# Kernel tuning notes

Hardware: AMD Instinct MI355X
Metric: run time of the kernel (lower is better)

## Reference

```python
import jax, jax.numpy as jnp
import numpy as np

B, S, DIM = 4, 2048, 1024
H, HD = 16, 64
MB = 16
NMB = S // MB
DEG, CP = 3, 8
NB = CP + DEG  # 11 basis functions
NKNOTS = CP + 1 + 2 * DEG  # 15
EPS = 1e-6
BASE_LR = 1.0


def bspline(x, knots, degree=DEG):
    # Cox-de Boor recursion; x: (...,), knots: (G,) uniform -> (..., G-1-degree)
    xk = x[..., None]
    G = knots.shape[0]
    b = ((xk >= knots[:-1]) & (xk < knots[1:])).astype(x.dtype)
    for k in range(1, degree + 1):
        left = (xk - knots[: G - 1 - k]) / (knots[k: G - 1] - knots[: G - 1 - k])
        right = (knots[k + 1: G] - xk) / (knots[k + 1: G] - knots[1: G - k])
        b = left * b[..., :-1] + right * b[..., 1:]
    return b


def ln_fwd(x, gamma, beta, eps=EPS):
    mu = x.mean(-1, keepdims=True)
    var = ((x - mu) ** 2).mean(-1, keepdims=True)
    x_hat = (x - mu) / jnp.sqrt(var + eps)
    return gamma * x_hat + beta


def ln_fused_l2_bwd(x, l2_target, gamma, beta, eps=EPS):
    mu = x.mean(-1, keepdims=True)
    var = ((x - mu) ** 2).mean(-1, keepdims=True)
    std = jnp.sqrt(var + eps)
    x_hat = (x - mu) / std
    grad_x_hat = (gamma * x_hat + beta - l2_target) * gamma
    z = (grad_x_hat - grad_x_hat.mean(-1, keepdims=True)
         - x_hat * (grad_x_hat * x_hat).mean(-1, keepdims=True)) / std
    return z


def apply_rope(t, ang):
    # t: (B,H,S,hd), ang: (S, hd//2) rotation angles
    cos, sin = jnp.cos(ang), jnp.sin(ang)
    t1, t2 = t[..., 0::2], t[..., 1::2]
    r1 = t1 * cos - t2 * sin
    r2 = t1 * sin + t2 * cos
    return jnp.stack([r1, r2], axis=-1).reshape(t.shape)


def setup_inputs() -> dict:
    key = jax.random.key(0)
    ks = jax.random.split(key, 8)
    s = 0.02
    x = jax.random.normal(ks[0], (B, S, DIM), dtype=jnp.float32)
    inv_freq = 1.0 / (10000.0 ** (jnp.arange(0, HD, 2, dtype=jnp.float32) / HD))
    pos_frequencies = jnp.arange(S, dtype=jnp.float32)[:, None] * inv_freq[None, :]
    Wq = jax.random.normal(ks[1], (DIM, DIM), dtype=jnp.float32) * s
    Wk = jax.random.normal(ks[2], (DIM, DIM), dtype=jnp.float32) * s
    Wv = jax.random.normal(ks[3], (DIM, DIM), dtype=jnp.float32) * s
    Wo = jax.random.normal(ks[4], (DIM, DIM), dtype=jnp.float32) * s
    lr_W = jax.random.normal(ks[5], (H, 1, DIM), dtype=jnp.float32) * s
    lr_b = jnp.zeros((H, 1), dtype=jnp.float32)
    g_scale = jnp.zeros((MB,), dtype=jnp.float32)
    ttt_gamma = jnp.ones((H, HD), dtype=jnp.float32)
    ttt_beta = jnp.zeros((H, HD), dtype=jnp.float32)
    post_w = jnp.ones((DIM,), dtype=jnp.float32)
    post_b = jnp.zeros((DIM,), dtype=jnp.float32)
    knots = jnp.linspace(-1.0, 1.0, NKNOTS, dtype=jnp.float32)
    coefficients = jax.random.normal(ks[6], (H, NB, HD), dtype=jnp.float32) * s
    return dict(x=x, pos_frequencies=pos_frequencies, Wq=Wq, Wk=Wk, Wv=Wv, Wo=Wo,
                lr_W=lr_W, lr_b=lr_b, g_scale=g_scale, ttt_gamma=ttt_gamma,
                ttt_beta=ttt_beta, post_w=post_w, post_b=post_b,
                coefficients=coefficients, knots=knots)


def reference(x, pos_frequencies, Wq, Wk, Wv, Wo, lr_W, lr_b, g_scale,
              ttt_gamma, ttt_beta, post_w, post_b, coefficients, knots):
    Bx, Sx = x.shape[:2]
    proj = lambda W: (x @ W.T).reshape(Bx, Sx, H, HD).transpose(0, 2, 1, 3)
    Q = apply_rope(proj(Wq), pos_frequencies)
    K = apply_rope(proj(Wk), pos_frequencies)
    V = apply_rope(proj(Wv), pos_frequencies)

    to_mb = lambda t: t.reshape(Bx, H, NMB, MB, HD).transpose(2, 0, 1, 3, 4)
    Qm, Km, Vm = to_mb(Q), to_mb(K), to_mb(V)  # (n,B,H,m,hd)

    # inner-loop learning rates (get_learning_rate)
    x4 = x.reshape(Bx, NMB, MB, DIM)
    lr = BASE_LR * jax.nn.sigmoid(
        jnp.einsum('bnkd,hd->bhnk', x4, lr_W[:, 0, :]) + lr_b.reshape(1, H, 1, 1)) / HD
    gs = jnp.clip(1.0 / jnp.arange(1, MB + 1, dtype=x.dtype) + g_scale, 0.0, None)
    eta = (lr * gs).transpose(2, 0, 1, 3)  # (n,B,H,m)

    gamma = ttt_gamma[None, :, None, :]
    beta = ttt_beta[None, :, None, :]
    W0 = jnp.broadcast_to(coefficients, (Bx, H, NB, HD))

    def step(W, inp):
        Qi, Ki, Vi, ei = inp  # (B,H,m,hd), eta (B,H,m)
        basK = bspline(Ki, knots)                      # (B,H,m,hd,nb)
        Zk = jax.nn.silu(Ki) + jnp.einsum('bhmdn,bhnd->bhmd', basK, W)
        gz = ln_fused_l2_bwd(Zk, Vi - Ki, gamma, beta)  # (B,H,m,hd)
        tok = jnp.einsum('bhm,bhmd,bhmdn->bhmnd', ei, gz, basK)
        cum = jnp.cumsum(tok, axis=2)                  # causal coeff-grad (B,H,m,nb,hd)
        basQ = bspline(Qi, knots)
        Zq = (jax.nn.silu(Qi)
              + jnp.einsum('bhmdn,bhnd->bhmd', basQ, W)
              - jnp.einsum('bhmdn,bhmnd->bhmd', basQ, cum))
        y = Qi + ln_fwd(Zq, gamma, beta)
        return W - cum[:, :, -1], y

    _, ys = jax.lax.scan(step, W0, (Qm, Km, Vm, eta))  # ys: (n,B,H,m,hd)
    out = ys.transpose(1, 0, 3, 2, 4).reshape(Bx, Sx, DIM)

    mu = out.mean(-1, keepdims=True)
    var = ((out - mu) ** 2).mean(-1, keepdims=True)
    out = (out - mu) / jnp.sqrt(var + EPS) * post_w + post_b
    return out @ Wo.T
```

## Files before the change

kernel.cpp:

```cpp
#include <hip/hip_runtime.h>
#include <stdint.h>


typedef unsigned short ushort_t;
typedef _Float16 f16x8 __attribute__((ext_vector_type(8)));
typedef float f32x4 __attribute__((ext_vector_type(4)));

__device__ __forceinline__ float fast_silu(float x) {
    const float e = __builtin_amdgcn_exp2f(-1.4426950408889634f * x);
    return x * __builtin_amdgcn_rcpf(1.0f + e);
}
__device__ __forceinline__ float fast_rsq(float x) {
    return __builtin_amdgcn_rsqf(x);
}

__device__ __forceinline__ void gl16(const ushort_t* g, ushort_t* l) {
    __builtin_amdgcn_global_load_lds(
        (const __attribute__((address_space(1))) void*)g,
        (__attribute__((address_space(3))) void*)l, 16, 0, 0);
}

template <int CTRL>
__device__ __forceinline__ float dpp_add(float v) {
    int p = __builtin_amdgcn_update_dpp(0, __float_as_int(v), CTRL, 0xF, 0xF, false);
    return v + __int_as_float(p);
}
__device__ __forceinline__ float wave_sum(float v) {
    v = dpp_add<0xB1>(v);
    v = dpp_add<0x4E>(v);
    v = dpp_add<0x141>(v);
    v = dpp_add<0x140>(v);
    v = dpp_add<0x142>(v);
    v = dpp_add<0x143>(v);
    return __int_as_float(__builtin_amdgcn_readlane(__float_as_int(v), 63));
}

__device__ __forceinline__ float rdl63(float v) {
    return __int_as_float(__builtin_amdgcn_readlane(__float_as_int(v), 63));
}

__device__ __forceinline__ void wave_sum6(float& s0, float& s1, float& s2,
                                          float& s3, float& s4, float& s5) {
    asm volatile(
        "s_nop 1\n\t"
        "v_add_f32_dpp %0, %0, %0 quad_perm:[1,0,3,2] row_mask:0xf bank_mask:0xf\n\t"
        "v_add_f32_dpp %1, %1, %1 quad_perm:[1,0,3,2] row_mask:0xf bank_mask:0xf\n\t"
        "v_add_f32_dpp %2, %2, %2 quad_perm:[1,0,3,2] row_mask:0xf bank_mask:0xf\n\t"
        "v_add_f32_dpp %3, %3, %3 quad_perm:[1,0,3,2] row_mask:0xf bank_mask:0xf\n\t"
        "v_add_f32_dpp %4, %4, %4 quad_perm:[1,0,3,2] row_mask:0xf bank_mask:0xf\n\t"
        "v_add_f32_dpp %5, %5, %5 quad_perm:[1,0,3,2] row_mask:0xf bank_mask:0xf\n\t"
        "v_add_f32_dpp %0, %0, %0 quad_perm:[2,3,0,1] row_mask:0xf bank_mask:0xf\n\t"
        "v_add_f32_dpp %1, %1, %1 quad_perm:[2,3,0,1] row_mask:0xf bank_mask:0xf\n\t"
        "v_add_f32_dpp %2, %2, %2 quad_perm:[2,3,0,1] row_mask:0xf bank_mask:0xf\n\t"
        "v_add_f32_dpp %3, %3, %3 quad_perm:[2,3,0,1] row_mask:0xf bank_mask:0xf\n\t"
        "v_add_f32_dpp %4, %4, %4 quad_perm:[2,3,0,1] row_mask:0xf bank_mask:0xf\n\t"
        "v_add_f32_dpp %5, %5, %5 quad_perm:[2,3,0,1] row_mask:0xf bank_mask:0xf\n\t"
        "v_add_f32_dpp %0, %0, %0 row_half_mirror row_mask:0xf bank_mask:0xf\n\t"
        "v_add_f32_dpp %1, %1, %1 row_half_mirror row_mask:0xf bank_mask:0xf\n\t"
        "v_add_f32_dpp %2, %2, %2 row_half_mirror row_mask:0xf bank_mask:0xf\n\t"
        "v_add_f32_dpp %3, %3, %3 row_half_mirror row_mask:0xf bank_mask:0xf\n\t"
        "v_add_f32_dpp %4, %4, %4 row_half_mirror row_mask:0xf bank_mask:0xf\n\t"
        "v_add_f32_dpp %5, %5, %5 row_half_mirror row_mask:0xf bank_mask:0xf\n\t"
        "v_add_f32_dpp %0, %0, %0 row_mirror row_mask:0xf bank_mask:0xf\n\t"
        "v_add_f32_dpp %1, %1, %1 row_mirror row_mask:0xf bank_mask:0xf\n\t"
        "v_add_f32_dpp %2, %2, %2 row_mirror row_mask:0xf bank_mask:0xf\n\t"
        "v_add_f32_dpp %3, %3, %3 row_mirror row_mask:0xf bank_mask:0xf\n\t"
        "v_add_f32_dpp %4, %4, %4 row_mirror row_mask:0xf bank_mask:0xf\n\t"
        "v_add_f32_dpp %5, %5, %5 row_mirror row_mask:0xf bank_mask:0xf\n\t"
        "v_add_f32_dpp %0, %0, %0 row_bcast:15 row_mask:0xf bank_mask:0xf bound_ctrl:0\n\t"
        "v_add_f32_dpp %1, %1, %1 row_bcast:15 row_mask:0xf bank_mask:0xf bound_ctrl:0\n\t"
        "v_add_f32_dpp %2, %2, %2 row_bcast:15 row_mask:0xf bank_mask:0xf bound_ctrl:0\n\t"
        "v_add_f32_dpp %3, %3, %3 row_bcast:15 row_mask:0xf bank_mask:0xf bound_ctrl:0\n\t"
        "v_add_f32_dpp %4, %4, %4 row_bcast:15 row_mask:0xf bank_mask:0xf bound_ctrl:0\n\t"
        "v_add_f32_dpp %5, %5, %5 row_bcast:15 row_mask:0xf bank_mask:0xf bound_ctrl:0\n\t"
        "v_add_f32_dpp %0, %0, %0 row_bcast:31 row_mask:0xf bank_mask:0xf bound_ctrl:0\n\t"
        "v_add_f32_dpp %1, %1, %1 row_bcast:31 row_mask:0xf bank_mask:0xf bound_ctrl:0\n\t"
        "v_add_f32_dpp %2, %2, %2 row_bcast:31 row_mask:0xf bank_mask:0xf bound_ctrl:0\n\t"
        "v_add_f32_dpp %3, %3, %3 row_bcast:31 row_mask:0xf bank_mask:0xf bound_ctrl:0\n\t"
        "v_add_f32_dpp %4, %4, %4 row_bcast:31 row_mask:0xf bank_mask:0xf bound_ctrl:0\n\t"
        "v_add_f32_dpp %5, %5, %5 row_bcast:31 row_mask:0xf bank_mask:0xf bound_ctrl:0"
        : "+v"(s0), "+v"(s1), "+v"(s2), "+v"(s3), "+v"(s4), "+v"(s5));
}

__device__ __forceinline__ void wave_sum2(float& s0, float& s1) {
    asm volatile(
        "s_nop 1\n\t"
        "v_add_f32_dpp %0, %0, %0 quad_perm:[1,0,3,2] row_mask:0xf bank_mask:0xf\n\t"
        "v_add_f32_dpp %1, %1, %1 quad_perm:[1,0,3,2] row_mask:0xf bank_mask:0xf\n\t"
        "s_nop 0\n\t"
        "v_add_f32_dpp %0, %0, %0 quad_perm:[2,3,0,1] row_mask:0xf bank_mask:0xf\n\t"
        "v_add_f32_dpp %1, %1, %1 quad_perm:[2,3,0,1] row_mask:0xf bank_mask:0xf\n\t"
        "s_nop 0\n\t"
        "v_add_f32_dpp %0, %0, %0 row_half_mirror row_mask:0xf bank_mask:0xf\n\t"
        "v_add_f32_dpp %1, %1, %1 row_half_mirror row_mask:0xf bank_mask:0xf\n\t"
        "s_nop 0\n\t"
        "v_add_f32_dpp %0, %0, %0 row_mirror row_mask:0xf bank_mask:0xf\n\t"
        "v_add_f32_dpp %1, %1, %1 row_mirror row_mask:0xf bank_mask:0xf\n\t"
        "s_nop 0\n\t"
        "v_add_f32_dpp %0, %0, %0 row_bcast:15 row_mask:0xf bank_mask:0xf bound_ctrl:0\n\t"
        "v_add_f32_dpp %1, %1, %1 row_bcast:15 row_mask:0xf bank_mask:0xf bound_ctrl:0\n\t"
        "s_nop 0\n\t"
        "v_add_f32_dpp %0, %0, %0 row_bcast:31 row_mask:0xf bank_mask:0xf bound_ctrl:0\n\t"
        "v_add_f32_dpp %1, %1, %1 row_bcast:31 row_mask:0xf bank_mask:0xf bound_ctrl:0"
        : "+v"(s0), "+v"(s1));
}

struct Bas4 { float n[4]; int row; };
__device__ __forceinline__ Bas4 bspline4(float x) {
    const float xp1 = x + 1.0f;
    const float s7 = xp1 * 7.0f;
    const float fi = floorf(s7);
    const bool valid = (fi >= 0.0f) && (fi <= 13.0f);
    const float fic = valid ? fi : 0.0f;
    const float t = s7 - fic;
    const float u = 1.0f - t;
    const float t2 = t * t;
    const float t3 = t2 * t;
    const float u3 = u * u * u;
    const float N0 = u3 * 0.16666666666666666f;
    const float N3 = t3 * 0.16666666666666666f;
    const float N1 = fmaf(0.5f, t3, 0.66666666666666666f - t2);
    const float N2 = 1.0f - N0 - N1 - N3;

    Bas4 r;
    const int i = (int)fic;
    const float nv[4] = {N0, N1, N2, N3};
#pragma unroll
    for (int tt = 0; tt < 4; ++tt) {
        const int j = i + tt - 3;
        const bool ok = valid && ((unsigned)j <= 10u);
        r.n[tt] = ok ? nv[tt] : 0.0f;
    }
    r.row = i;
    return r;
}

__device__ __forceinline__ void split16_body(
    const float* __restrict__ in, ushort_t* __restrict__ hi,
    ushort_t* __restrict__ lo, int i)
{
    const float4 f = reinterpret_cast<const float4*>(in)[i];
    union { _Float16 h[4]; ushort4 u; } hv, lv;
    hv.h[0] = (_Float16)f.x; hv.h[1] = (_Float16)f.y;
    hv.h[2] = (_Float16)f.z; hv.h[3] = (_Float16)f.w;
    lv.h[0] = (_Float16)(f.x - (float)hv.h[0]);
    lv.h[1] = (_Float16)(f.y - (float)hv.h[1]);
    lv.h[2] = (_Float16)(f.z - (float)hv.h[2]);
    lv.h[3] = (_Float16)(f.w - (float)hv.h[3]);
    reinterpret_cast<ushort4*>(hi)[i] = hv.u;
    reinterpret_cast<ushort4*>(lo)[i] = lv.u;
}

__device__ __forceinline__ void cast16_body(
    const float* __restrict__ in, ushort_t* __restrict__ out, int i)
{
    const float4 f = reinterpret_cast<const float4*>(in)[i];
    union { _Float16 h[4]; ushort4 u; } cv;
    cv.h[0] = (_Float16)f.x; cv.h[1] = (_Float16)f.y;
    cv.h[2] = (_Float16)f.z; cv.h[3] = (_Float16)f.w;
    reinterpret_cast<ushort4*>(out)[i] = cv.u;
}

__global__ __launch_bounds__(256) void prep_kernel(
    const float* __restrict__ x,
    const float* __restrict__ Wq, const float* __restrict__ Wk,
    const float* __restrict__ Wv,
    const float* __restrict__ lrW, const float* __restrict__ lrb,
    const float* __restrict__ gsc, const float* __restrict__ posf,
    ushort_t* __restrict__ xh, ushort_t* __restrict__ xl,
    ushort_t* __restrict__ Wq16, ushort_t* __restrict__ Wk16,
    ushort_t* __restrict__ Wv16,
    float* __restrict__ eta, float2* __restrict__ rtab)
{
    const int bid = blockIdx.x;
    const int tid = threadIdx.x;
    if (bid < 8192) {
        split16_body(x, xh, xl, bid * 256 + tid);
    } else if (bid < 9216) {
        cast16_body(Wq, Wq16, (bid - 8192) * 256 + tid);
    } else if (bid < 10240) {
        cast16_body(Wk, Wk16, (bid - 9216) * 256 + tid);
    } else if (bid < 11264) {
        cast16_body(Wv, Wv16, (bid - 10240) * 256 + tid);
    } else if (bid < 13312) {
        const int row = (bid - 11264) * 4 + (tid >> 6);
        const int lane = tid & 63;
        float xv[16];
#pragma unroll
        for (int i = 0; i < 16; ++i) xv[i] = x[(size_t)row * 1024 + lane + i * 64];
        const int b = row >> 11, s = row & 2047, n = s >> 4, m = s & 15;
        const float gs = fmaxf(1.0f / (float)(m + 1) + gsc[m], 0.0f);
        for (int h = 0; h < 16; ++h) {
            float acc = 0.0f;
#pragma unroll
            for (int i = 0; i < 16; ++i) acc += xv[i] * lrW[h * 1024 + lane + i * 64];
            acc = wave_sum(acc);
            if (lane == 0) {
                float sig = 1.0f / (1.0f + expf(-(acc + lrb[h])));
                eta[(((size_t)(b * 16 + h)) * 128 + n) * 16 + m] = (sig / 64.0f) * gs;
            }
        }
    } else {
        const int i = (bid - 13312) * 256 + tid;
        const float ang = posf[i];
        rtab[i] = make_float2(cosf(ang), sinf(ang));
    }
}

__global__ __launch_bounds__(256) void cast16_kernel(
    const float* __restrict__ in, ushort_t* __restrict__ out, int n4)
{
    const int i = blockIdx.x * 256 + threadIdx.x;
    if (i >= n4) return;
    cast16_body(in, out, i);
}

#define RAW_BAR()                                                              \
    __builtin_amdgcn_s_barrier();                                              \
    asm volatile("" ::: "memory");

__global__ __launch_bounds__(512) void qkv_rope_kernel(
    const ushort_t* __restrict__ xh, const ushort_t* __restrict__ xl,
    const ushort_t* __restrict__ Wq16, const ushort_t* __restrict__ Wk16,
    const ushort_t* __restrict__ Wv16,
    const float2* __restrict__ tab,
    float* __restrict__ Qb, float* __restrict__ Kb, float* __restrict__ Vb)
{
    const int cid = blockIdx.y * 64 + blockIdx.x;
    const int swz = (cid & 7) * 192 + (cid >> 3);
    const int rowbase = (swz & 63) * 128;
    const int colbase = (swz >> 6) * 128;
    const int sel = colbase >> 10;
    const ushort_t* WB = (sel == 0) ? Wq16 : (sel == 1) ? Wk16 : Wv16;
    float* dst = (sel == 0) ? Qb : (sel == 1) ? Kb : Vb;
    const int colm = colbase & 1023;

    __shared__ __align__(16) ushort_t Ash[3][4096];
    __shared__ __align__(16) ushort_t Asl[3][4096];
    __shared__ __align__(16) ushort_t Bsh[3][4096];
    const int tid = threadIdx.x;
    const int wv = tid >> 6, ln = tid & 63;
    const int l15 = ln & 15, lq = ln >> 4;
    const int lsw = lq ^ ((l15 >> 1) & 3);
    const int wm = wv >> 2, wn = wv & 3;
    const int srow = tid >> 2;
    const int skseg = (((tid & 3) ^ ((srow >> 1) & 3)) * 8);
    const ushort_t* gA_h = xh + (size_t)(rowbase + srow) * 1024 + skseg;
    const ushort_t* gA_l = xl + (size_t)(rowbase + srow) * 1024 + skseg;
    const ushort_t* gB   = WB + (size_t)(colm + srow) * 1024 + skseg;
    const int wlds = wv * 512;
    f32x4 acc[4][2] = {};

    ushort_t *cAh = &Ash[0][0], *cAl = &Asl[0][0], *cB = &Bsh[0][0];
    ushort_t *nAh = &Ash[1][0], *nAl = &Asl[1][0], *nB = &Bsh[1][0];
    ushort_t *pAh = &Ash[2][0], *pAl = &Asl[2][0], *pB = &Bsh[2][0];

    gl16(gA_h + 0,  cAh + wlds); gl16(gA_l + 0,  cAl + wlds); gl16(gB + 0,  cB + wlds);
    gl16(gA_h + 32, nAh + wlds); gl16(gA_l + 32, nAl + wlds); gl16(gB + 32, nB + wlds);

    for (int p = 0; p < 32; ++p) {
        const int kn = (p + 2) * 32;
        if (kn < 1024) {
            gl16(gA_h + kn, pAh + wlds);
            gl16(gA_l + kn, pAl + wlds);
            gl16(gB + kn,   pB + wlds);
            asm volatile("s_waitcnt vmcnt(6)" ::: "memory");
        } else if (p == 30) {
            asm volatile("s_waitcnt vmcnt(3)" ::: "memory");
        } else {
            asm volatile("s_waitcnt vmcnt(0)" ::: "memory");
        }
        RAW_BAR()
        {
            f16x8 bh[2];
#pragma unroll
            for (int u = 0; u < 2; ++u) {
                const int br = (wn * 32 + u * 16 + l15) * 32 + lsw * 8;
                bh[u] = *reinterpret_cast<const f16x8*>(&cB[br]);
            }
#pragma unroll
            for (int t = 0; t < 4; ++t) {
                const int ar = (wm * 64 + t * 16 + l15) * 32 + lsw * 8;
                const f16x8 ah = *reinterpret_cast<const f16x8*>(&cAh[ar]);
                const f16x8 al = *reinterpret_cast<const f16x8*>(&cAl[ar]);
#pragma unroll
                for (int u = 0; u < 2; ++u) {
                    acc[t][u] = __builtin_amdgcn_mfma_f32_16x16x32_f16(ah, bh[u], acc[t][u], 0, 0, 0);
                    acc[t][u] = __builtin_amdgcn_mfma_f32_16x16x32_f16(al, bh[u], acc[t][u], 0, 0, 0);
                }
            }
        }
        RAW_BAR()
        ushort_t* t0;
        t0 = cAh; cAh = nAh; nAh = pAh; pAh = t0;
        t0 = cAl; cAl = nAl; nAl = pAl; pAl = t0;
        t0 = cB;  cB  = nB;  nB  = pB;  pB  = t0;
    }

#pragma unroll
    for (int t = 0; t < 4; ++t)
#pragma unroll
        for (int u = 0; u < 2; ++u) {
            const int col = colm + wn * 32 + u * 16 + l15;
            const int d = col & 63, h = col >> 6;
            const int angidx = d >> 1;
            const int odd = d & 1;
#pragma unroll
            for (int r = 0; r < 4; ++r) {
                const int row = rowbase + wm * 64 + t * 16 + lq * 4 + r;
                const int b = row >> 11, s = row & 2047;
                const float2 cs = tab[s * 32 + angidx];
                const float own = acc[t][u][r];
                const float partner = __shfl_xor(own, 1, 64);
                const float res = odd ? (partner * cs.y + own * cs.x)
                                      : (own * cs.x - partner * cs.y);
                const int n = s >> 4, m = s & 15;
                dst[(((size_t)(b * 16 + h)) * 128 + n) * 1024 + m * 64 + d] = res;
            }
        }
}

__global__ __launch_bounds__(1024) void scan_kernel(
    const float* __restrict__ Qb, const float* __restrict__ Kb,
    const float* __restrict__ Vb, const float* __restrict__ eta,
    const float* __restrict__ tg, const float* __restrict__ tb,
    const float* __restrict__ coeff, float* __restrict__ out_pre)
{
    __shared__ __align__(16) float Wl[17 * 64];
    __shared__ __align__(16) float cum[16 * 17 * 64];
    __shared__ __align__(16) float Ucum[16 * 17 * 64];

    const int tid = threadIdx.x;
    const int m = tid >> 6, d = tid & 63;
    const int b = blockIdx.x >> 4, h = blockIdx.x & 15;

    const float gam = tg[h * 64 + d];
    const float bet = tb[h * 64 + d];
    const float gam2 = gam * gam;
    const float G = wave_sum(gam2);

    for (int i = tid; i < 1088; i += 1024)
        Wl[i] = (i >= 192 && i < 896) ? coeff[h * 704 + (i - 192)] : 0.0f;
    {
        const float4 z = {0.0f, 0.0f, 0.0f, 0.0f};
        float4* c4 = (float4*)cum;
        float4* u4 = (float4*)Ucum;
        for (int i = tid; i < 4352; i += 1024) { c4[i] = z; u4[i] = z; }
    }
    __syncthreads();

    const size_t base = ((size_t)(b * 16 + h)) * 131072;
    const float* Qp = Qb + base;
    const float* Kp = Kb + base;
    const float* Vp = Vb + base;
    const float* ep = eta + ((size_t)(b * 16 + h)) * 2048;

    float kf = Kp[tid], vf = Vp[tid], qf = Qp[tid], ei = ep[m];
    int rprev = 0;
    const int cb = m * 1088 + d;

    Bas4 bk = bspline4(kf);
    float szk = fast_silu(kf);
    float E = gam * (bet - (vf - kf));

    for (int n = 0; n < 128; ++n) {
        const int n1 = (n < 127) ? n + 1 : n;
        const float kfN = Kp[n1 * 1024 + tid];
        const float vfN = Vp[n1 * 1024 + tid];
        const float qfN = Qp[n1 * 1024 + tid];
        const float eiN = ep[n1 * 16 + m];

        float zk = szk;
        {
            const float* w = &Wl[bk.row * 64 + d];
            zk = fmaf(bk.n[0], w[0],   zk);
            zk = fmaf(bk.n[1], w[64],  zk);
            zk = fmaf(bk.n[2], w[128], zk);
            zk = fmaf(bk.n[3], w[192], zk);
        }

        float s0 = zk, s1 = zk * zk, s2 = gam2 * zk,
              s3 = gam2 * (zk * zk), s4 = E, s5 = E * zk;
        wave_sum6(s0, s1, s2, s3, s4, s5);
        const float r0 = rdl63(s0);
        const float r1 = rdl63(s1);
        const float r2 = rdl63(s2);
        const float r3 = rdl63(s3);
        const float r4 = rdl63(s4);
        const float r5 = rdl63(s5);

        const float mu = r0 * (1.0f / 64.0f);
        const float var = r1 * (1.0f / 64.0f) - mu * mu;
        const float rstd = fast_rsq(var + 1e-6f);
        const float xhat = (zk - mu) * rstd;
        const float gxh = gam2 * xhat + E;
        const float t1 = rstd * (r2 - mu * G) + r4;
        const float t2 = rstd * rstd * (r3 - 2.0f * mu * r2 + mu * mu * G)
                       + rstd * (r5 - mu * r4);
        const float gz = (gxh - t1 * (1.0f / 64.0f) - xhat * (t2 * (1.0f / 64.0f))) * rstd;

        const float tokf = ei * gz;
        {
            float* cz = &cum[cb + rprev * 64];
            cz[0] = 0.0f; cz[64] = 0.0f; cz[128] = 0.0f; cz[192] = 0.0f;
            float* cw = &cum[cb + bk.row * 64];
            cw[0]   = tokf * bk.n[0];
            cw[64]  = tokf * bk.n[1];
            cw[128] = tokf * bk.n[2];
            cw[192] = tokf * bk.n[3];
            rprev = bk.row;
        }
        __syncthreads();

        if (tid < 176) {
            float4* c4 = (float4*)cum;
            float4* u4 = (float4*)Ucum;
            float4* w4 = (float4*)Wl;
            float4 v[16];
#pragma unroll
            for (int mm = 0; mm < 16; ++mm) v[mm] = c4[mm * 272 + 48 + tid];
            float4 a = w4[48 + tid];
#pragma unroll
            for (int mm = 0; mm < 16; ++mm) {
                a.x -= v[mm].x; a.y -= v[mm].y; a.z -= v[mm].z; a.w -= v[mm].w;
                u4[mm * 272 + 48 + tid] = a;
            }
            w4[48 + tid] = a;
        }
        const Bas4 bq = bspline4(qf);
        float zq = fast_silu(qf);
        const Bas4 bkN = bspline4(kfN);
        const float szkN = fast_silu(kfN);
        const float EN = gam * (bet - (vfN - kfN));
        __syncthreads();

        {
            const float* u = &Ucum[cb + bq.row * 64];
            zq = fmaf(bq.n[0], u[0],   zq);
            zq = fmaf(bq.n[1], u[64],  zq);
            zq = fmaf(bq.n[2], u[128], zq);
            zq = fmaf(bq.n[3], u[192], zq);
        }

        float q0 = zq, q1 = zq * zq;
        wave_sum2(q0, q1);
        const float u1 = rdl63(q0);
        const float u2 = rdl63(q1);
        const float mu2 = u1 * (1.0f / 64.0f);
        const float var2 = u2 * (1.0f / 64.0f) - mu2 * mu2;
        const float rstd2 = fast_rsq(var2 + 1e-6f);
        const float y = qf + gam * (zq - mu2) * rstd2 + bet;
        out_pre[((size_t)b * 2048 + n * 16 + m) * 1024 + h * 64 + d] = y;

        kf = kfN; vf = vfN; qf = qfN; ei = eiN;
        bk = bkN; szk = szkN; E = EN;
    }
}

__global__ __launch_bounds__(256) void ln_kernel(
    const float* __restrict__ in, const float* __restrict__ pw,
    const float* __restrict__ pb, ushort_t* __restrict__ o16)
{
    const int row = blockIdx.x * 4 + (threadIdx.x >> 6);
    const int lane = threadIdx.x & 63;
    const float* r = in + (size_t)row * 1024;
    float v[16];
    float s1 = 0.0f, s2 = 0.0f;
#pragma unroll
    for (int i = 0; i < 16; ++i) {
        v[i] = r[lane + i * 64];
        s1 += v[i];
        s2 += v[i] * v[i];
    }
    s1 = wave_sum(s1);
    s2 = wave_sum(s2);
    const float mu = s1 * (1.0f / 1024.0f);
    const float var = s2 * (1.0f / 1024.0f) - mu * mu;
    const float rstd = rsqrtf(var + 1e-6f);
#pragma unroll
    for (int i = 0; i < 16; ++i) {
        const int c = lane + i * 64;
        const float o = (v[i] - mu) * rstd * pw[c] + pb[c];
        union { _Float16 h; ushort_t u; } cv;
        cv.h = (_Float16)o;
        o16[(size_t)row * 1024 + c] = cv.u;
    }
}

__global__ __launch_bounds__(512) void out_gemm_kernel(
    const ushort_t* __restrict__ Ag, const ushort_t* __restrict__ Bg,
    float* __restrict__ out)
{
    const int cid = blockIdx.y * 64 + blockIdx.x;
    const int swz = (cid & 7) * 64 + (cid >> 3);
    const int rowbase = (swz & 63) * 128;
    const int colbase = (swz >> 6) * 128;

    __shared__ __align__(16) ushort_t Ash[2][4096];
    __shared__ __align__(16) ushort_t Bsh[2][4096];
    const int tid = threadIdx.x;
    const int wv = tid >> 6, ln = tid & 63;
    const int l15 = ln & 15, lq = ln >> 4;
    const int lsw = lq ^ ((l15 >> 1) & 3);
    const int wm = wv >> 2, wn = wv & 3;
    const int srow = tid >> 2;
    const int skseg = (((tid & 3) ^ ((srow >> 1) & 3)) * 8);
    const ushort_t* gA = Ag + (size_t)(rowbase + srow) * 1024 + skseg;
    const ushort_t* gB = Bg + (size_t)(colbase + srow) * 1024 + skseg;
    const int wlds = wv * 512;
    f32x4 acc[4][2] = {};

#define OG_STAGE(B, KO)                                                        \
    gl16(gA + (KO), &Ash[B][wlds]);                                            \
    gl16(gB + (KO), &Bsh[B][wlds]);

#define OG_COMPUTE(B)                                                          \
    {                                                                          \
        f16x8 bh[2];                                                           \
        _Pragma("unroll")                                                      \
        for (int u = 0; u < 2; ++u) {                                          \
            const int br = (wn * 32 + u * 16 + l15) * 32 + lsw * 8;            \
            bh[u] = *reinterpret_cast<const f16x8*>(&Bsh[B][br]);              \
        }                                                                      \
        _Pragma("unroll")                                                      \
        for (int t = 0; t < 4; ++t) {                                          \
            const int ar = (wm * 64 + t * 16 + l15) * 32 + lsw * 8;            \
            const f16x8 ah = *reinterpret_cast<const f16x8*>(&Ash[B][ar]);     \
            _Pragma("unroll")                                                  \
            for (int u = 0; u < 2; ++u)                                        \
                acc[t][u] = __builtin_amdgcn_mfma_f32_16x16x32_f16(ah, bh[u], acc[t][u], 0, 0, 0); \
        }                                                                      \
    }

    OG_STAGE(0, 0)
    for (int k0 = 0; k0 < 1024; k0 += 64) {
        OG_STAGE(1, k0 + 32)
        asm volatile("s_waitcnt vmcnt(2)" ::: "memory");
        RAW_BAR()
        OG_COMPUTE(0)
        RAW_BAR()
        if (k0 + 64 < 1024) {
            OG_STAGE(0, k0 + 64)
            asm volatile("s_waitcnt vmcnt(2)" ::: "memory");
        } else {
            asm volatile("s_waitcnt vmcnt(0)" ::: "memory");
        }
        RAW_BAR()
        OG_COMPUTE(1)
        RAW_BAR()
    }
#undef OG_STAGE
#undef OG_COMPUTE

#pragma unroll
    for (int t = 0; t < 4; ++t)
#pragma unroll
        for (int u = 0; u < 2; ++u) {
            const int col = colbase + wn * 32 + u * 16 + l15;
#pragma unroll
            for (int r = 0; r < 4; ++r) {
                const int row = rowbase + wm * 64 + t * 16 + lq * 4 + r;
                out[(size_t)row * 1024 + col] = acc[t][u][r];
            }
        }
}

extern "C" void kernel_launch(void* const* d_in, const int* in_sizes, int n_in,
                              void* d_out, int out_size, void* d_ws, size_t ws_size,
                              hipStream_t stream) {
    const float* x    = (const float*)d_in[0];
    const float* posf = (const float*)d_in[1];
    const float* Wq   = (const float*)d_in[2];
    const float* Wk   = (const float*)d_in[3];
    const float* Wv   = (const float*)d_in[4];
    const float* Wo   = (const float*)d_in[5];
    const float* lrW  = (const float*)d_in[6];
    const float* lrb  = (const float*)d_in[7];
    const float* gsc  = (const float*)d_in[8];
    const float* tg   = (const float*)d_in[9];
    const float* tb   = (const float*)d_in[10];
    const float* pw   = (const float*)d_in[11];
    const float* pb   = (const float*)d_in[12];
    const float* coeff= (const float*)d_in[13];

    char* ws = (char*)d_ws;
    float*    Qb   = (float*)(ws);
    float*    Kb   = (float*)(ws + 33554432);
    float*    Vb   = (float*)(ws + 67108864);
    ushort_t* xh   = (ushort_t*)(ws + 100663296);
    ushort_t* xl   = (ushort_t*)(ws + 117440512);
    float*    outp = (float*)(ws + 100663296);
    float*    eta  = (float*)(ws + 134217728);
    ushort_t* Wq16 = (ushort_t*)(ws + 134742016);
    ushort_t* Wk16 = (ushort_t*)(ws + 136839168);
    ushort_t* Wv16 = (ushort_t*)(ws + 138936320);
    ushort_t* Wo16 = (ushort_t*)(ws + 147324928);
    ushort_t* ln16 = (ushort_t*)(ws);
    float2*   rtab = (float2*)(ws + 147324928);

    prep_kernel<<<13568, 256, 0, stream>>>(x, Wq, Wk, Wv, lrW, lrb, gsc, posf,
                                           xh, xl, Wq16, Wk16, Wv16, eta, rtab);
    qkv_rope_kernel<<<dim3(64, 24), 512, 0, stream>>>(xh, xl, Wq16, Wk16, Wv16,
                                                      rtab, Qb, Kb, Vb);
    cast16_kernel<<<1024, 256, 0, stream>>>(Wo, Wo16, 262144);
    scan_kernel<<<64, 1024, 0, stream>>>(Qb, Kb, Vb, eta, tg, tb, coeff, outp);
    ln_kernel<<<2048, 256, 0, stream>>>(outp, pw, pb, ln16);
    out_gemm_kernel<<<dim3(64, 8), 512, 0, stream>>>(ln16, Wo16, (float*)d_out);
}
```

Before: 537.0 us.

## Drop hi/lo split of x in QKV GEMM and use BK=64 double-buffered tiles

The QKV projection used to split x into fp16 hi and lo parts and issue two MFMAs per tile to keep near-fp32 accuracy. It now casts x to a single fp16 array, which halves the A-operand traffic and the MFMA count. Both the QKV and output GEMMs now share a double-buffered pipeline with a 64-wide K step and a new XOR swizzle, giving fewer barriers per K. The cost is lower precision in Q/K/V, which feed a recurrent scan where errors can compound, plus a change in LDS footprint.

```diff
diff --git a/kernel.cpp b/kernel.cpp
--- a/kernel.cpp
+++ b/kernel.cpp
@@ -135,22 +135,6 @@
     return r;
 }
 
-__device__ __forceinline__ void split16_body(
-    const float* __restrict__ in, ushort_t* __restrict__ hi,
-    ushort_t* __restrict__ lo, int i)
-{
-    const float4 f = reinterpret_cast<const float4*>(in)[i];
-    union { _Float16 h[4]; ushort4 u; } hv, lv;
-    hv.h[0] = (_Float16)f.x; hv.h[1] = (_Float16)f.y;
-    hv.h[2] = (_Float16)f.z; hv.h[3] = (_Float16)f.w;
-    lv.h[0] = (_Float16)(f.x - (float)hv.h[0]);
-    lv.h[1] = (_Float16)(f.y - (float)hv.h[1]);
-    lv.h[2] = (_Float16)(f.z - (float)hv.h[2]);
-    lv.h[3] = (_Float16)(f.w - (float)hv.h[3]);
-    reinterpret_cast<ushort4*>(hi)[i] = hv.u;
-    reinterpret_cast<ushort4*>(lo)[i] = lv.u;
-}
-
 __device__ __forceinline__ void cast16_body(
     const float* __restrict__ in, ushort_t* __restrict__ out, int i)
 {
@@ -167,7 +151,7 @@
     const float* __restrict__ Wv,
     const float* __restrict__ lrW, const float* __restrict__ lrb,
     const float* __restrict__ gsc, const float* __restrict__ posf,
-    ushort_t* __restrict__ xh, ushort_t* __restrict__ xl,
+    ushort_t* __restrict__ x16,
     ushort_t* __restrict__ Wq16, ushort_t* __restrict__ Wk16,
     ushort_t* __restrict__ Wv16,
     float* __restrict__ eta, float2* __restrict__ rtab)
@@ -175,7 +159,7 @@
     const int bid = blockIdx.x;
     const int tid = threadIdx.x;
     if (bid < 8192) {
-        split16_body(x, xh, xl, bid * 256 + tid);
+        cast16_body(x, x16, bid * 256 + tid);
     } else if (bid < 9216) {
         cast16_body(Wq, Wq16, (bid - 8192) * 256 + tid);
     } else if (bid < 10240) {
@@ -219,8 +203,61 @@
     __builtin_amdgcn_s_barrier();                                              \
     asm volatile("" ::: "memory");
 
+#define G2_DECLS()                                                             \
+    const int tid = threadIdx.x;                                               \
+    const int wv = tid >> 6, ln = tid & 63;                                    \
+    const int l15 = ln & 15, lq = ln >> 4, l7 = ln & 7;                        \
+    const int wm = wv >> 2, wn = wv & 3;                                       \
+    const int r8 = ln >> 3;                          \
+    const int gsw = (l7 ^ r8) * 8;                   \
+    const int a0d = (wv * 8) * 64;                 \
+    const int a1d = (64 + wv * 8) * 64;                                        \
+    f32x4 acc[4][2] = {};
+
+#define G2_STAGE(buf, KO)                                                      \
+    gl16(gA0 + (KO), &As[buf][a0d]);                                           \
+    gl16(gA1 + (KO), &As[buf][a1d]);                                           \
+    gl16(gB0 + (KO), &Bs[buf][a0d]);                                           \
+    gl16(gB1 + (KO), &Bs[buf][a1d]);
+
+#define G2_COMPUTE(buf)                                                        \
+    _Pragma("unroll")                                                          \
+    for (int ks = 0; ks < 2; ++ks) {                                           \
+        f16x8 bh[2];                                                           \
+        _Pragma("unroll")                                                      \
+        for (int u = 0; u < 2; ++u) {                                          \
+            const int br = (wn * 32 + u * 16 + l15) * 64                       \
+                         + ((((ks << 2) + lq) ^ l7) << 3);                     \
+            bh[u] = *reinterpret_cast<const f16x8*>(&Bs[buf][br]);             \
+        }                                                                      \
+        _Pragma("unroll")                                                      \
+        for (int t = 0; t < 4; ++t) {                                          \
+            const int ar = (wm * 64 + t * 16 + l15) * 64                       \
+                         + ((((ks << 2) + lq) ^ l7) << 3);                     \
+            const f16x8 ah = *reinterpret_cast<const f16x8*>(&As[buf][ar]);    \
+            _Pragma("unroll")                                                  \
+            for (int u = 0; u < 2; ++u)                                        \
+                acc[t][u] = __builtin_amdgcn_mfma_f32_16x16x32_f16(ah, bh[u], acc[t][u], 0, 0, 0); \
+        }                                                                      \
+    }
+
+#define G2_LOOP()                                                              \
+    G2_STAGE(0, 0)                                                             \
+    for (int p = 0; p < 16; ++p) {                                             \
+        const int buf = p & 1;                                                 \
+        if (p < 15) {                                                          \
+            G2_STAGE(buf ^ 1, (p + 1) * 64)                                    \
+            asm volatile("s_waitcnt vmcnt(4)" ::: "memory");                   \
+        } else {                                                               \
+            asm volatile("s_waitcnt vmcnt(0)" ::: "memory");                   \
+        }                                                                      \
+        RAW_BAR()                                                              \
+        G2_COMPUTE(buf)                                                        \
+        RAW_BAR()                                                              \
+    }
+
 __global__ __launch_bounds__(512) void qkv_rope_kernel(
-    const ushort_t* __restrict__ xh, const ushort_t* __restrict__ xl,
+    const ushort_t* __restrict__ x16,
     const ushort_t* __restrict__ Wq16, const ushort_t* __restrict__ Wk16,
     const ushort_t* __restrict__ Wv16,
     const float2* __restrict__ tab,
@@ -235,67 +272,15 @@
     float* dst = (sel == 0) ? Qb : (sel == 1) ? Kb : Vb;
     const int colm = colbase & 1023;
 
-    __shared__ __align__(16) ushort_t Ash[3][4096];
-    __shared__ __align__(16) ushort_t Asl[3][4096];
-    __shared__ __align__(16) ushort_t Bsh[3][4096];
-    const int tid = threadIdx.x;
-    const int wv = tid >> 6, ln = tid & 63;
-    const int l15 = ln & 15, lq = ln >> 4;
-    const int lsw = lq ^ ((l15 >> 1) & 3);
-    const int wm = wv >> 2, wn = wv & 3;
-    const int srow = tid >> 2;
-    const int skseg = (((tid & 3) ^ ((srow >> 1) & 3)) * 8);
-    const ushort_t* gA_h = xh + (size_t)(rowbase + srow) * 1024 + skseg;
-    const ushort_t* gA_l = xl + (size_t)(rowbase + srow) * 1024 + skseg;
-    const ushort_t* gB   = WB + (size_t)(colm + srow) * 1024 + skseg;
-    const int wlds = wv * 512;
-    f32x4 acc[4][2] = {};
-
-    ushort_t *cAh = &Ash[0][0], *cAl = &Asl[0][0], *cB = &Bsh[0][0];
-    ushort_t *nAh = &Ash[1][0], *nAl = &Asl[1][0], *nB = &Bsh[1][0];
-    ushort_t *pAh = &Ash[2][0], *pAl = &Asl[2][0], *pB = &Bsh[2][0];
-
-    gl16(gA_h + 0,  cAh + wlds); gl16(gA_l + 0,  cAl + wlds); gl16(gB + 0,  cB + wlds);
-    gl16(gA_h + 32, nAh + wlds); gl16(gA_l + 32, nAl + wlds); gl16(gB + 32, nB + wlds);
-
-    for (int p = 0; p < 32; ++p) {
-        const int kn = (p + 2) * 32;
-        if (kn < 1024) {
-            gl16(gA_h + kn, pAh + wlds);
-            gl16(gA_l + kn, pAl + wlds);
-            gl16(gB + kn,   pB + wlds);
-            asm volatile("s_waitcnt vmcnt(6)" ::: "memory");
-        } else if (p == 30) {
-            asm volatile("s_waitcnt vmcnt(3)" ::: "memory");
-        } else {
-            asm volatile("s_waitcnt vmcnt(0)" ::: "memory");
-        }
-        RAW_BAR()
-        {
-            f16x8 bh[2];
-#pragma unroll
-            for (int u = 0; u < 2; ++u) {
-                const int br = (wn * 32 + u * 16 + l15) * 32 + lsw * 8;
-                bh[u] = *reinterpret_cast<const f16x8*>(&cB[br]);
-            }
-#pragma unroll
-            for (int t = 0; t < 4; ++t) {
-                const int ar = (wm * 64 + t * 16 + l15) * 32 + lsw * 8;
-                const f16x8 ah = *reinterpret_cast<const f16x8*>(&cAh[ar]);
-                const f16x8 al = *reinterpret_cast<const f16x8*>(&cAl[ar]);
-#pragma unroll
-                for (int u = 0; u < 2; ++u) {
-                    acc[t][u] = __builtin_amdgcn_mfma_f32_16x16x32_f16(ah, bh[u], acc[t][u], 0, 0, 0);
-                    acc[t][u] = __builtin_amdgcn_mfma_f32_16x16x32_f16(al, bh[u], acc[t][u], 0, 0, 0);
-                }
-            }
-        }
-        RAW_BAR()
-        ushort_t* t0;
-        t0 = cAh; cAh = nAh; nAh = pAh; pAh = t0;
-        t0 = cAl; cAl = nAl; nAl = pAl; pAl = t0;
-        t0 = cB;  cB  = nB;  nB  = pB;  pB  = t0;
-    }
+    __shared__ __align__(16) ushort_t As[2][8192];
+    __shared__ __align__(16) ushort_t Bs[2][8192];
+    G2_DECLS()
+    const ushort_t* gA0 = x16 + (size_t)(rowbase + wv * 8 + r8) * 1024 + gsw;
+    const ushort_t* gA1 = gA0 + (size_t)64 * 1024;
+    const ushort_t* gB0 = WB + (size_t)(colm + wv * 8 + r8) * 1024 + gsw;
+    const ushort_t* gB1 = gB0 + (size_t)64 * 1024;
+
+    G2_LOOP()
 
 #pragma unroll
     for (int t = 0; t < 4; ++t)
@@ -496,61 +481,15 @@
     const int rowbase = (swz & 63) * 128;
     const int colbase = (swz >> 6) * 128;
 
-    __shared__ __align__(16) ushort_t Ash[2][4096];
-    __shared__ __align__(16) ushort_t Bsh[2][4096];
-    const int tid = threadIdx.x;
-    const int wv = tid >> 6, ln = tid & 63;
-    const int l15 = ln & 15, lq = ln >> 4;
-    const int lsw = lq ^ ((l15 >> 1) & 3);
-    const int wm = wv >> 2, wn = wv & 3;
-    const int srow = tid >> 2;
-    const int skseg = (((tid & 3) ^ ((srow >> 1) & 3)) * 8);
-    const ushort_t* gA = Ag + (size_t)(rowbase + srow) * 1024 + skseg;
-    const ushort_t* gB = Bg + (size_t)(colbase + srow) * 1024 + skseg;
-    const int wlds = wv * 512;
-    f32x4 acc[4][2] = {};
-
-#define OG_STAGE(B, KO)                                                        \
-    gl16(gA + (KO), &Ash[B][wlds]);                                            \
-    gl16(gB + (KO), &Bsh[B][wlds]);
-
-#define OG_COMPUTE(B)                                                          \
-    {                                                                          \
-        f16x8 bh[2];                                                           \
-        _Pragma("unroll")                                                      \
-        for (int u = 0; u < 2; ++u) {                                          \
-            const int br = (wn * 32 + u * 16 + l15) * 32 + lsw * 8;            \
-            bh[u] = *reinterpret_cast<const f16x8*>(&Bsh[B][br]);              \
-        }                                                                      \
-        _Pragma("unroll")                                                      \
-        for (int t = 0; t < 4; ++t) {                                          \
-            const int ar = (wm * 64 + t * 16 + l15) * 32 + lsw * 8;            \
-            const f16x8 ah = *reinterpret_cast<const f16x8*>(&Ash[B][ar]);     \
-            _Pragma("unroll")                                                  \
-            for (int u = 0; u < 2; ++u)                                        \
-                acc[t][u] = __builtin_amdgcn_mfma_f32_16x16x32_f16(ah, bh[u], acc[t][u], 0, 0, 0); \
-        }                                                                      \
-    }
-
-    OG_STAGE(0, 0)
-    for (int k0 = 0; k0 < 1024; k0 += 64) {
-        OG_STAGE(1, k0 + 32)
-        asm volatile("s_waitcnt vmcnt(2)" ::: "memory");
-        RAW_BAR()
-        OG_COMPUTE(0)
-        RAW_BAR()
-        if (k0 + 64 < 1024) {
-            OG_STAGE(0, k0 + 64)
-            asm volatile("s_waitcnt vmcnt(2)" ::: "memory");
-        } else {
-            asm volatile("s_waitcnt vmcnt(0)" ::: "memory");
-        }
-        RAW_BAR()
-        OG_COMPUTE(1)
-        RAW_BAR()
-    }
-#undef OG_STAGE
-#undef OG_COMPUTE
+    __shared__ __align__(16) ushort_t As[2][8192];
+    __shared__ __align__(16) ushort_t Bs[2][8192];
+    G2_DECLS()
+    const ushort_t* gA0 = Ag + (size_t)(rowbase + wv * 8 + r8) * 1024 + gsw;
+    const ushort_t* gA1 = gA0 + (size_t)64 * 1024;
+    const ushort_t* gB0 = Bg + (size_t)(colbase + wv * 8 + r8) * 1024 + gsw;
+    const ushort_t* gB1 = gB0 + (size_t)64 * 1024;
+
+    G2_LOOP()
 
 #pragma unroll
     for (int t = 0; t < 4; ++t)
@@ -587,8 +526,7 @@
     float*    Qb   = (float*)(ws);
     float*    Kb   = (float*)(ws + 33554432);
     float*    Vb   = (float*)(ws + 67108864);
-    ushort_t* xh   = (ushort_t*)(ws + 100663296);
-    ushort_t* xl   = (ushort_t*)(ws + 117440512);
+    ushort_t* x16  = (ushort_t*)(ws + 100663296);
     float*    outp = (float*)(ws + 100663296);
     float*    eta  = (float*)(ws + 134217728);
     ushort_t* Wq16 = (ushort_t*)(ws + 134742016);
@@ -599,8 +537,8 @@
     float2*   rtab = (float2*)(ws + 147324928);
 
     prep_kernel<<<13568, 256, 0, stream>>>(x, Wq, Wk, Wv, lrW, lrb, gsc, posf,
-                                           xh, xl, Wq16, Wk16, Wv16, eta, rtab);
-    qkv_rope_kernel<<<dim3(64, 24), 512, 0, stream>>>(xh, xl, Wq16, Wk16, Wv16,
+                                           x16, Wq16, Wk16, Wv16, eta, rtab);
+    qkv_rope_kernel<<<dim3(64, 24), 512, 0, stream>>>(x16, Wq16, Wk16, Wv16,
                                                       rtab, Qb, Kb, Vb);
     cast16_kernel<<<1024, 256, 0, stream>>>(Wo, Wo16, 262144);
     scan_kernel<<<64, 1024, 0, stream>>>(Qb, Kb, Vb, eta, tg, tb, coeff, outp);
```

Result: faster. 497.6 us (-7.3%).
